# Kernel tuning notes

Hardware: AMD Instinct MI355X
Metric: run time of the kernel (lower is better)

Reference implementation:

```python
import jax, jax.numpy as jnp
import numpy as np

H = 16  # head_count
NEG = -1e18

def setup_inputs() -> dict:
    key = jax.random.key(0)
    ks = jax.random.split(key, 8)
    B, L, D = 4, 2048, 1024
    s = 1.0 / np.sqrt(D)
    return {
        "key":   jax.random.normal(ks[0], (B, L, D), jnp.float32),
        "value": jax.random.normal(ks[1], (B, L, D), jnp.float32),
        "query": jax.random.normal(ks[2], (B, L, D), jnp.float32),
        "mask":  jax.random.randint(ks[3], (B, L, L), 0, 2).astype(bool),
        "Wk": jax.random.normal(ks[4], (D, D), jnp.float32) * s,
        "bk": jnp.zeros((D,), jnp.float32),
        "Wv": jax.random.normal(ks[5], (D, D), jnp.float32) * s,
        "bv": jnp.zeros((D,), jnp.float32),
        "Wq": jax.random.normal(ks[6], (D, D), jnp.float32) * s,
        "bq": jnp.zeros((D,), jnp.float32),
        "Wo": jax.random.normal(ks[7], (D, D), jnp.float32) * s,
        "bo": jnp.zeros((D,), jnp.float32),
    }

def reference(key, value, query, mask, Wk, bk, Wv, bv, Wq, bq, Wo, bo):
    B, Lk, D = key.shape
    Lq = query.shape[1]
    dh = D // H

    def shape(x, L):  # (B, L, D) -> (B, H, L, dh)
        return x.reshape(B, L, H, dh).transpose(0, 2, 1, 3)

    k = shape(key @ Wk + bk, Lk)
    v = shape(value @ Wv + bv, Lk)
    q = shape(query @ Wq + bq, Lq) / jnp.sqrt(jnp.asarray(dh, query.dtype))

    scores = jnp.einsum('bhqd,bhkd->bhqk', q, k).astype(jnp.float32)
    scores = jnp.where(mask[:, None, :, :], NEG, scores)  # masked_fill
    attn = jax.nn.softmax(scores, axis=-1).astype(q.dtype)
    # dropout is identity at inference
    ctx = jnp.einsum('bhqk,bhkd->bhqd', attn, v)
    ctx = ctx.transpose(0, 2, 1, 3).reshape(B, Lq, D)  # unshape
    output = ctx @ Wo + bo
    top_attn = attn[:, 0, :, :]
    return (output, top_attn)
```

## Files before the change

kernel.cpp:

```cpp
#include <hip/hip_runtime.h>
#include <hip/hip_bf16.h>
#include <stdint.h>

#define Bn 4
#define Ln 2048
#define Dn 1024
#define Hn 16
#define DHn 64

typedef __attribute__((ext_vector_type(8))) short short8;
typedef __attribute__((ext_vector_type(4))) float f32x4;
typedef unsigned long long u64;
typedef __hip_bfloat16 bf16;

union U8 { uint32_t u[4]; short8 s; };

__device__ __forceinline__ short f2b(float x) {
  bf16 b = __float2bfloat16(x);
  return *(short*)&b;
}

__device__ __forceinline__ uint32_t cvt_pk_bf16(float lo, float hi) {
  uint32_t r;
  asm("v_cvt_pk_bf16_f32 %0, %1, %2" : "=v"(r) : "v"(lo), "v"(hi));
  return r;
}

__device__ __forceinline__ void gll16(const void* g, void* l) {
  __builtin_amdgcn_global_load_lds(
      (const __attribute__((address_space(1))) void*)g,
      (__attribute__((address_space(3))) void*)l, 16, 0, 0);
}

__global__ __launch_bounds__(256) void f32_to_bf16_3(
    const float* __restrict__ A, const float* __restrict__ B2, const float* __restrict__ C3,
    short* __restrict__ oA, short* __restrict__ oB, short* __restrict__ oC, int n4)
{
  const int z = blockIdx.y;
  const float* in = (z == 0) ? A : (z == 1) ? B2 : C3;
  short* out = (z == 0) ? oA : (z == 1) ? oB : oC;
  int i = blockIdx.x * 256 + threadIdx.x;
  if (i < n4) {
    float4 v = ((const float4*)in)[i];
    short4 o;
    o.x = f2b(v.x); o.y = f2b(v.y); o.z = f2b(v.z); o.w = f2b(v.w);
    ((short4*)out)[i] = o;
  }
}

__global__ __launch_bounds__(256) void transpose_w_bf16(
    const float* __restrict__ W0, const float* __restrict__ W1,
    const float* __restrict__ W2, const float* __restrict__ W3,
    short* __restrict__ WT0, short* __restrict__ WT1,
    short* __restrict__ WT2, short* __restrict__ WT3)
{
  __shared__ float t[64][65];
  const int z = blockIdx.z;
  const float* src = (z == 0) ? W0 : (z == 1) ? W1 : (z == 2) ? W2 : W3;
  short* dst = (z == 0) ? WT0 : (z == 1) ? WT1 : (z == 2) ? WT2 : WT3;
  const int tid = threadIdx.x;
  const int k0 = blockIdx.x * 64, n0 = blockIdx.y * 64;
  #pragma unroll
  for (int it = 0; it < 4; ++it) {
    int idx = it * 256 + tid;
    int row = idx >> 4, c4 = (idx & 15) * 4;
    *(float4*)&t[row][c4] = *(const float4*)&src[(size_t)(k0 + row) * Dn + n0 + c4];
  }
  __syncthreads();
  #pragma unroll
  for (int it = 0; it < 4; ++it) {
    int idx = it * 256 + tid;
    int nr = idx >> 4, kc = (idx & 15) * 4;
    short4 o;
    o.x = f2b(t[kc + 0][nr]); o.y = f2b(t[kc + 1][nr]);
    o.z = f2b(t[kc + 2][nr]); o.w = f2b(t[kc + 3][nr]);
    *(short4*)&dst[(size_t)(n0 + nr) * Dn + k0 + kc] = o;
  }
}

__global__ __launch_bounds__(256) void gemm_bias_bf16(
    const short* __restrict__ Xs, const short* __restrict__ WTs,
    const float* __restrict__ bias, void* __restrict__ Cout,
    int M, int N, int K, float scale, int mode)
{
  __shared__ short lds[2 * 128 * 32];
  short* ldsA = lds;
  short* ldsB = lds + 128 * 32;
  const int tid  = threadIdx.x;
  const int lane = tid & 63;
  const int wv   = tid >> 6;
  const int quad = lane >> 4;
  const int l16  = lane & 15;
  const int m0 = blockIdx.y * 128, n0 = blockIdx.x * 128;
  const int wm = (wv >> 1) * 64, wn = (wv & 1) * 64;

  f32x4 acc[4][4];
  #pragma unroll
  for (int i = 0; i < 4; ++i)
    #pragma unroll
    for (int j = 0; j < 4; ++j)
      acc[i][j] = (f32x4){0.f, 0.f, 0.f, 0.f};

  for (int k0 = 0; k0 < K; k0 += 32) {
    __syncthreads();
    #pragma unroll
    for (int r = 0; r < 2; ++r) {
      int idx = r * 256 + tid;
      int row = idx >> 2, kc = idx & 3;
      gll16(Xs  + (size_t)(m0 + row) * K + k0 + kc * 8, ldsA + idx * 8);
      gll16(WTs + (size_t)(n0 + row) * K + k0 + kc * 8, ldsB + idx * 8);
    }
    __syncthreads();
    short8 af[4], bfr[4];
    #pragma unroll
    for (int i = 0; i < 4; ++i)
      af[i] = *(const short8*)(ldsA + (wm + i * 16 + l16) * 32 + quad * 8);
    #pragma unroll
    for (int j = 0; j < 4; ++j)
      bfr[j] = *(const short8*)(ldsB + (wn + j * 16 + l16) * 32 + quad * 8);
    #pragma unroll
    for (int i = 0; i < 4; ++i)
      #pragma unroll
      for (int j = 0; j < 4; ++j)
        acc[i][j] = __builtin_amdgcn_mfma_f32_16x16x32_bf16(af[i], bfr[j], acc[i][j], 0, 0, 0);
  }

  if (mode == 0) {
    float* C = (float*)Cout;
    #pragma unroll
    for (int j = 0; j < 4; ++j) {
      int n = n0 + wn + j * 16 + l16;
      float bv = bias[n];
      #pragma unroll
      for (int i = 0; i < 4; ++i) {
        int mb = m0 + wm + i * 16 + quad * 4;
        #pragma unroll
        for (int r = 0; r < 4; ++r)
          C[(size_t)(mb + r) * N + n] = (acc[i][j][r] + bv) * scale;
      }
    }
  } else if (mode == 1) {
    short* C = (short*)Cout;
    #pragma unroll
    for (int j = 0; j < 4; ++j) {
      int n = n0 + wn + j * 16 + l16;
      float bv = bias[n];
      #pragma unroll
      for (int i = 0; i < 4; ++i) {
        int mb = m0 + wm + i * 16 + quad * 4;
        #pragma unroll
        for (int r = 0; r < 4; ++r)
          C[(size_t)(mb + r) * N + n] = f2b((acc[i][j][r] + bv) * scale);
      }
    }
  } else {
    short* C = (short*)Cout;
    #pragma unroll
    for (int j = 0; j < 4; ++j) {
      int n = n0 + wn + j * 16 + l16;
      float bv = bias[n];
      int hh = n >> 6, dd = n & 63;
      #pragma unroll
      for (int i = 0; i < 4; ++i) {
        int mb = m0 + wm + i * 16 + quad * 4;
        int bb = mb >> 11, ll = mb & 2047;
        short4 o;
        o.x = f2b((acc[i][j][0] + bv) * scale);
        o.y = f2b((acc[i][j][1] + bv) * scale);
        o.z = f2b((acc[i][j][2] + bv) * scale);
        o.w = f2b((acc[i][j][3] + bv) * scale);
        *(short4*)&C[((size_t)(bb * 16 + hh) * 64 + dd) * 2048 + ll] = o;
      }
    }
  }
}

__global__ __launch_bounds__(256) void pack_mask(const int* __restrict__ mask, u64* __restrict__ pm)
{
  size_t tg = (size_t)blockIdx.x * 256 + threadIdx.x;
  int v = mask[tg];
  u64 bal = __ballot(v != 0);
  if ((threadIdx.x & 63) == 0) pm[tg >> 6] = bal;
}


__device__ __forceinline__ const short8* ldsfrag(const short* lds, int row, int colb) {
  return (const short8*)((const char*)lds + row * 128 + (colb ^ ((row & 7) << 4)));
}

__global__ __launch_bounds__(256) void attn_fused(
    const short* __restrict__ qb, const short* __restrict__ kb,
    const short* __restrict__ vT, const u64* __restrict__ pm,
    short* __restrict__ ctx_bf, float* __restrict__ topattn)
{
  __shared__ short ldsK[64 * 64];
  __shared__ short ldsVT[64 * 64];
  const int tid  = threadIdx.x;
  const int lane = tid & 63, wv = tid >> 6;
  const int quad = lane >> 4, l16 = lane & 15;
  const int b = blockIdx.z, h = blockIdx.y, q0 = blockIdx.x * 64;
  const int q_g = q0 + wv * 16 + l16;

  const short* qrow = qb + (size_t)(b * Ln + q_g) * Dn + h * DHn;
  short8 qf[2];
  qf[0] = *(const short8*)(qrow + quad * 8);
  qf[1] = *(const short8*)(qrow + 32 + quad * 8);

  const u64* pmq = pm + (size_t)(b * Ln + q_g) * 32;
  const short* kbase = kb + (size_t)b * Ln * Dn + h * DHn;
  const short* vbase = vT + (size_t)(b * Hn + h) * DHn * Ln;

  float m_r = -INFINITY, l_r = 0.f;
  f32x4 oc[4];
  #pragma unroll
  for (int dt = 0; dt < 4; ++dt) oc[dt] = (f32x4){0.f, 0.f, 0.f, 0.f};

  const int srcA = ((lane >> 4) & 1) * 32 + l16;
  const int srcB = srcA + 16;
  const bool hiHalf = (lane & 32) != 0;

  for (int k0 = 0; k0 < Ln; k0 += 64) {
    __syncthreads();
    #pragma unroll
    for (int it = 0; it < 2; ++it) {
      int idx = it * 256 + tid;
      int row = idx >> 3, cb = (idx & 7) * 16;
      int scb = cb ^ ((row & 7) << 4);
      gll16(kbase + (size_t)(k0 + row) * Dn + (scb >> 1), ldsK + idx * 8);
      gll16(vbase + (size_t)row * Ln + k0 + (scb >> 1), ldsVT + idx * 8);
    }
    __syncthreads();

    f32x4 sv[4];
    #pragma unroll
    for (int mt = 0; mt < 4; ++mt) sv[mt] = (f32x4){0.f, 0.f, 0.f, 0.f};
    #pragma unroll
    for (int s = 0; s < 2; ++s)
      #pragma unroll
      for (int mt = 0; mt < 4; ++mt) {
        short8 kf = *ldsfrag(ldsK, mt * 16 + l16, s * 64 + quad * 16);
        sv[mt] = __builtin_amdgcn_mfma_f32_16x16x32_bf16(kf, qf[s], sv[mt], 0, 0, 0);
      }

    u64 w = pmq[k0 >> 6];
    float ps[4][4];
    float tm = -INFINITY;
    #pragma unroll
    for (int mt = 0; mt < 4; ++mt)
      #pragma unroll
      for (int r = 0; r < 4; ++r) {
        int kl = mt * 16 + quad * 4 + r;
        float s = ((w >> kl) & 1ull) ? -INFINITY : sv[mt][r];
        ps[mt][r] = s;
        tm = fmaxf(tm, s);
      }
    tm = fmaxf(tm, __shfl_xor(tm, 16, 64));
    tm = fmaxf(tm, __shfl_xor(tm, 32, 64));
    if (tm > m_r + 8.f) {
      float sc = __expf(m_r - tm);
      l_r *= sc;
      #pragma unroll
      for (int dt = 0; dt < 4; ++dt)
        #pragma unroll
        for (int r = 0; r < 4; ++r) oc[dt][r] *= sc;
      m_r = tm;
    }
    float ls = 0.f;
    #pragma unroll
    for (int mt = 0; mt < 4; ++mt)
      #pragma unroll
      for (int r = 0; r < 4; ++r) {
        float p = __expf(ps[mt][r] - m_r);
        ps[mt][r] = p;
        ls += p;
      }
    l_r += ls;

    uint32_t d0[4], d1[4];
    #pragma unroll
    for (int mt = 0; mt < 4; ++mt) {
      d0[mt] = cvt_pk_bf16(ps[mt][0], ps[mt][1]);
      d1[mt] = cvt_pk_bf16(ps[mt][2], ps[mt][3]);
    }

    #pragma unroll
    for (int ks = 0; ks < 2; ++ks) {
      uint32_t a0  = (uint32_t)__shfl((int)d0[2 * ks],     srcA, 64);
      uint32_t a0b = (uint32_t)__shfl((int)d0[2 * ks + 1], srcA, 64);
      uint32_t a1  = (uint32_t)__shfl((int)d1[2 * ks],     srcA, 64);
      uint32_t a1b = (uint32_t)__shfl((int)d1[2 * ks + 1], srcA, 64);
      uint32_t b0  = (uint32_t)__shfl((int)d0[2 * ks],     srcB, 64);
      uint32_t b0b = (uint32_t)__shfl((int)d0[2 * ks + 1], srcB, 64);
      uint32_t b1  = (uint32_t)__shfl((int)d1[2 * ks],     srcB, 64);
      uint32_t b1b = (uint32_t)__shfl((int)d1[2 * ks + 1], srcB, 64);
      U8 u;
      u.u[0] = hiHalf ? a0b : a0;
      u.u[1] = hiHalf ? a1b : a1;
      u.u[2] = hiHalf ? b0b : b0;
      u.u[3] = hiHalf ? b1b : b1;
      short8 pf = u.s;
      #pragma unroll
      for (int dt = 0; dt < 4; ++dt) {
        short8 vf = *ldsfrag(ldsVT, dt * 16 + l16, ks * 64 + quad * 16);
        oc[dt] = __builtin_amdgcn_mfma_f32_16x16x32_bf16(vf, pf, oc[dt], 0, 0, 0);
      }
    }
  }

  l_r += __shfl_xor(l_r, 16, 64);
  l_r += __shfl_xor(l_r, 32, 64);
  const float rinv = (l_r > 0.f) ? 1.f / l_r : 0.f;

  short* crow = ctx_bf + (size_t)(b * Ln + q_g) * Dn + h * DHn;
  #pragma unroll
  for (int dt = 0; dt < 4; ++dt) {
    short4 o;
    o.x = f2b(oc[dt][0] * rinv); o.y = f2b(oc[dt][1] * rinv);
    o.z = f2b(oc[dt][2] * rinv); o.w = f2b(oc[dt][3] * rinv);
    *(short4*)&crow[dt * 16 + quad * 4] = o;
  }

  if (h == 0) {
    float* tpb = topattn + (size_t)(b * Ln + q_g) * Ln;
    for (int k0 = 0; k0 < Ln; k0 += 64) {
      __syncthreads();
      #pragma unroll
      for (int it = 0; it < 2; ++it) {
        int idx = it * 256 + tid;
        int row = idx >> 3, cb = (idx & 7) * 16;
        int scb = cb ^ ((row & 7) << 4);
        gll16(kbase + (size_t)(k0 + row) * Dn + (scb >> 1), ldsK + idx * 8);
      }
      __syncthreads();
      f32x4 sv[4];
      #pragma unroll
      for (int mt = 0; mt < 4; ++mt) sv[mt] = (f32x4){0.f, 0.f, 0.f, 0.f};
      #pragma unroll
      for (int s = 0; s < 2; ++s)
        #pragma unroll
        for (int mt = 0; mt < 4; ++mt) {
          short8 kf = *ldsfrag(ldsK, mt * 16 + l16, s * 64 + quad * 16);
          sv[mt] = __builtin_amdgcn_mfma_f32_16x16x32_bf16(kf, qf[s], sv[mt], 0, 0, 0);
        }
      u64 w = pmq[k0 >> 6];
      #pragma unroll
      for (int mt = 0; mt < 4; ++mt)
        #pragma unroll
        for (int r = 0; r < 4; ++r) {
          int kl = mt * 16 + quad * 4 + r;
          float p = ((w >> kl) & 1ull) ? 0.f : __expf(sv[mt][r] - m_r) * rinv;
          tpb[k0 + kl] = p;
        }
    }
  }
}

extern "C" void kernel_launch(void* const* d_in, const int* in_sizes, int n_in,
                              void* d_out, int out_size, void* d_ws, size_t ws_size,
                              hipStream_t stream) {
  (void)in_sizes; (void)n_in; (void)out_size; (void)ws_size;
  const float* key   = (const float*)d_in[0];
  const float* value = (const float*)d_in[1];
  const float* query = (const float*)d_in[2];
  const int*   mask  = (const int*)d_in[3];
  const float* Wk = (const float*)d_in[4];
  const float* bk = (const float*)d_in[5];
  const float* Wv = (const float*)d_in[6];
  const float* bv = (const float*)d_in[7];
  const float* Wq = (const float*)d_in[8];
  const float* bq = (const float*)d_in[9];
  const float* Wo = (const float*)d_in[10];
  const float* bo = (const float*)d_in[11];

  char* ws = (char*)d_ws;
  const size_t MiB = 1ull << 20;
  short* kc  = (short*)(ws +   0 * MiB);
  short* vc  = (short*)(ws +  16 * MiB);
  short* qc  = (short*)(ws +  32 * MiB);
  short* WkT = (short*)(ws +  48 * MiB);
  short* WvT = (short*)(ws +  50 * MiB);
  short* WqT = (short*)(ws +  52 * MiB);
  short* WoT = (short*)(ws +  54 * MiB);
  short* qb  = (short*)(ws +  56 * MiB);
  short* kb  = (short*)(ws +  72 * MiB);
  short* vT  = (short*)(ws +  88 * MiB);
  u64*   pm  = (u64*)  (ws + 104 * MiB);
  short* ctx_bf = (short*)(ws + 106 * MiB);

  float* out     = (float*)d_out;
  float* topattn = out + (size_t)Bn * Ln * Dn;

  const int M = Bn * Ln;
  const int n4 = (M * Dn) / 4;

  f32_to_bf16_3<<<dim3(n4 / 256, 3), 256, 0, stream>>>(key, value, query, kc, vc, qc, n4);
  transpose_w_bf16<<<dim3(16, 16, 4), 256, 0, stream>>>(Wk, Wv, Wq, Wo, WkT, WvT, WqT, WoT);

  gemm_bias_bf16<<<dim3(8, 64), 256, 0, stream>>>(kc, WkT, bk, kb, M, Dn, Dn, 1.0f,   1);
  gemm_bias_bf16<<<dim3(8, 64), 256, 0, stream>>>(vc, WvT, bv, vT, M, Dn, Dn, 1.0f,   2);
  gemm_bias_bf16<<<dim3(8, 64), 256, 0, stream>>>(qc, WqT, bq, qb, M, Dn, Dn, 0.125f, 1);

  pack_mask<<<dim3((Bn * Ln * Ln) / 256), 256, 0, stream>>>(mask, pm);

  attn_fused<<<dim3(Ln / 64, Hn, Bn), 256, 0, stream>>>(qb, kb, vT, pm, ctx_bf, topattn);

  gemm_bias_bf16<<<dim3(8, 64), 256, 0, stream>>>(ctx_bf, WoT, bo, out, M, Dn, Dn, 1.0f, 0);
}
```

Before: 593.6 us.

## Double-buffer GEMM and attention loads, fuse QKV GEMMs, inline top-attn write

The GEMM core and the attention kernel now double-buffer their LDS tiles, prefetching the next K-slice while computing the current one, and raise wave priority around MFMA blocks. The three QKV projections become one launch with a z dimension. The head-0 second pass that recomputed scores for top_attn is removed: probabilities are written during the main pass with per-tile maxima, and a small fix-up kernel rescales them by the final max and normalizer. The attention grid is remapped to a 1D swizzle that groups heads and batches. This costs extra LDS, a small extra kernel, and an extra read-modify-write over the top_attn buffer.

```diff
diff --git a/kernel.cpp b/kernel.cpp
--- a/kernel.cpp
+++ b/kernel.cpp
@@ -78,14 +78,12 @@
   }
 }
 
-__global__ __launch_bounds__(256) void gemm_bias_bf16(
+__device__ __forceinline__ void gemm_core(
     const short* __restrict__ Xs, const short* __restrict__ WTs,
     const float* __restrict__ bias, void* __restrict__ Cout,
     int M, int N, int K, float scale, int mode)
 {
-  __shared__ short lds[2 * 128 * 32];
-  short* ldsA = lds;
-  short* ldsB = lds + 128 * 32;
+  __shared__ short lds[2][2 * 128 * 32];
   const int tid  = threadIdx.x;
   const int lane = tid & 63;
   const int wv   = tid >> 6;
@@ -101,16 +99,30 @@
     for (int j = 0; j < 4; ++j)
       acc[i][j] = (f32x4){0.f, 0.f, 0.f, 0.f};
 
-  for (int k0 = 0; k0 < K; k0 += 32) {
-    __syncthreads();
-    #pragma unroll
-    for (int r = 0; r < 2; ++r) {
-      int idx = r * 256 + tid;
-      int row = idx >> 2, kc = idx & 3;
-      gll16(Xs  + (size_t)(m0 + row) * K + k0 + kc * 8, ldsA + idx * 8);
-      gll16(WTs + (size_t)(n0 + row) * K + k0 + kc * 8, ldsB + idx * 8);
-    }
-    __syncthreads();
+  #pragma unroll
+  for (int r = 0; r < 2; ++r) {
+    int idx = r * 256 + tid;
+    int row = idx >> 2, kc = idx & 3;
+    gll16(Xs  + (size_t)(m0 + row) * K + kc * 8, &lds[0][idx * 8]);
+    gll16(WTs + (size_t)(n0 + row) * K + kc * 8, &lds[0][128 * 32 + idx * 8]);
+  }
+  __syncthreads();
+
+  const int NT = K >> 5;
+  int cur = 0;
+  for (int t = 0; t < NT; ++t) {
+    if (t + 1 < NT) {
+      const int kn = (t + 1) * 32;
+      #pragma unroll
+      for (int r = 0; r < 2; ++r) {
+        int idx = r * 256 + tid;
+        int row = idx >> 2, kc = idx & 3;
+        gll16(Xs  + (size_t)(m0 + row) * K + kn + kc * 8, &lds[cur ^ 1][idx * 8]);
+        gll16(WTs + (size_t)(n0 + row) * K + kn + kc * 8, &lds[cur ^ 1][128 * 32 + idx * 8]);
+      }
+    }
+    const short* ldsA = lds[cur];
+    const short* ldsB = lds[cur] + 128 * 32;
     short8 af[4], bfr[4];
     #pragma unroll
     for (int i = 0; i < 4; ++i)
@@ -118,11 +130,15 @@
     #pragma unroll
     for (int j = 0; j < 4; ++j)
       bfr[j] = *(const short8*)(ldsB + (wn + j * 16 + l16) * 32 + quad * 8);
+    __builtin_amdgcn_s_setprio(1);
     #pragma unroll
     for (int i = 0; i < 4; ++i)
       #pragma unroll
       for (int j = 0; j < 4; ++j)
         acc[i][j] = __builtin_amdgcn_mfma_f32_16x16x32_bf16(af[i], bfr[j], acc[i][j], 0, 0, 0);
+    __builtin_amdgcn_s_setprio(0);
+    __syncthreads();
+    cur ^= 1;
   }
 
   if (mode == 0) {
@@ -175,6 +191,29 @@
   }
 }
 
+__global__ __launch_bounds__(256) void gemm_qkv(
+    const short* __restrict__ kc, const short* __restrict__ vc, const short* __restrict__ qc,
+    const short* __restrict__ WkT, const short* __restrict__ WvT, const short* __restrict__ WqT,
+    const float* __restrict__ bk, const float* __restrict__ bv, const float* __restrict__ bq,
+    short* __restrict__ kb, short* __restrict__ vT, short* __restrict__ qb2)
+{
+  const int z = blockIdx.z;
+  const short* Xs = (z == 0) ? kc : (z == 1) ? vc : qc;
+  const short* WT = (z == 0) ? WkT : (z == 1) ? WvT : WqT;
+  const float* bs = (z == 0) ? bk : (z == 1) ? bv : bq;
+  void* C = (z == 0) ? (void*)kb : (z == 1) ? (void*)vT : (void*)qb2;
+  float scale = (z == 2) ? 0.125f : 1.0f;
+  int mode = (z == 1) ? 2 : 1;
+  gemm_core(Xs, WT, bs, C, Bn * Ln, Dn, Dn, scale, mode);
+}
+
+__global__ __launch_bounds__(256) void gemm_wo(
+    const short* __restrict__ ctx, const short* __restrict__ WoT,
+    const float* __restrict__ bo, float* __restrict__ out)
+{
+  gemm_core(ctx, WoT, bo, out, Bn * Ln, Dn, Dn, 1.0f, 0);
+}
+
 __global__ __launch_bounds__(256) void pack_mask(const int* __restrict__ mask, u64* __restrict__ pm)
 {
   size_t tg = (size_t)blockIdx.x * 256 + threadIdx.x;
@@ -191,14 +230,19 @@
 __global__ __launch_bounds__(256) void attn_fused(
     const short* __restrict__ qb, const short* __restrict__ kb,
     const short* __restrict__ vT, const u64* __restrict__ pm,
-    short* __restrict__ ctx_bf, float* __restrict__ topattn)
-{
-  __shared__ short ldsK[64 * 64];
-  __shared__ short ldsVT[64 * 64];
+    short* __restrict__ ctx_bf, float* __restrict__ topattn,
+    float* __restrict__ mtile, float2* __restrict__ stat2)
+{
+  __shared__ short ldsK[2][64 * 64];
+  __shared__ short ldsVT[2][64 * 64];
   const int tid  = threadIdx.x;
   const int lane = tid & 63, wv = tid >> 6;
   const int quad = lane >> 4, l16 = lane & 15;
-  const int b = blockIdx.z, h = blockIdx.y, q0 = blockIdx.x * 64;
+  const int g = blockIdx.x;
+  const int x = (g >> 3) & 31;
+  const int c = (g & 7) + ((g >> 8) << 3);
+  const int h = c & 15, b = c >> 4;
+  const int q0 = x * 64;
   const int q_g = q0 + wv * 16 + l16;
 
   const short* qrow = qb + (size_t)(b * Ln + q_g) * Dn + h * DHn;
@@ -210,6 +254,16 @@
   const short* kbase = kb + (size_t)b * Ln * Dn + h * DHn;
   const short* vbase = vT + (size_t)(b * Hn + h) * DHn * Ln;
 
+  #pragma unroll
+  for (int it = 0; it < 2; ++it) {
+    int idx = it * 256 + tid;
+    int row = idx >> 3, cb = (idx & 7) * 16;
+    int scb = cb ^ ((row & 7) << 4);
+    gll16(kbase + (size_t)row * Dn + (scb >> 1), &ldsK[0][idx * 8]);
+    gll16(vbase + (size_t)row * Ln + (scb >> 1), &ldsVT[0][idx * 8]);
+  }
+  __syncthreads();
+
   float m_r = -INFINITY, l_r = 0.f;
   f32x4 oc[4];
   #pragma unroll
@@ -219,41 +273,38 @@
   const int srcB = srcA + 16;
   const bool hiHalf = (lane & 32) != 0;
 
-  for (int k0 = 0; k0 < Ln; k0 += 64) {
-    __syncthreads();
-    #pragma unroll
-    for (int it = 0; it < 2; ++it) {
-      int idx = it * 256 + tid;
-      int row = idx >> 3, cb = (idx & 7) * 16;
-      int scb = cb ^ ((row & 7) << 4);
-      gll16(kbase + (size_t)(k0 + row) * Dn + (scb >> 1), ldsK + idx * 8);
-      gll16(vbase + (size_t)row * Ln + k0 + (scb >> 1), ldsVT + idx * 8);
-    }
-    __syncthreads();
+  int cur = 0;
+  for (int t = 0; t < 32; ++t) {
+    const int k0 = t * 64;
+    if (t < 31) {
+      const int kn = k0 + 64;
+      #pragma unroll
+      for (int it = 0; it < 2; ++it) {
+        int idx = it * 256 + tid;
+        int row = idx >> 3, cb = (idx & 7) * 16;
+        int scb = cb ^ ((row & 7) << 4);
+        gll16(kbase + (size_t)(kn + row) * Dn + (scb >> 1), &ldsK[cur ^ 1][idx * 8]);
+        gll16(vbase + (size_t)row * Ln + kn + (scb >> 1), &ldsVT[cur ^ 1][idx * 8]);
+      }
+    }
 
     f32x4 sv[4];
     #pragma unroll
     for (int mt = 0; mt < 4; ++mt) sv[mt] = (f32x4){0.f, 0.f, 0.f, 0.f};
+    __builtin_amdgcn_s_setprio(1);
     #pragma unroll
     for (int s = 0; s < 2; ++s)
       #pragma unroll
       for (int mt = 0; mt < 4; ++mt) {
-        short8 kf = *ldsfrag(ldsK, mt * 16 + l16, s * 64 + quad * 16);
+        short8 kf = *ldsfrag(&ldsK[cur][0], mt * 16 + l16, s * 64 + quad * 16);
         sv[mt] = __builtin_amdgcn_mfma_f32_16x16x32_bf16(kf, qf[s], sv[mt], 0, 0, 0);
       }
-
-    u64 w = pmq[k0 >> 6];
-    float ps[4][4];
-    float tm = -INFINITY;
-    #pragma unroll
-    for (int mt = 0; mt < 4; ++mt)
-      #pragma unroll
-      for (int r = 0; r < 4; ++r) {
-        int kl = mt * 16 + quad * 4 + r;
-        float s = ((w >> kl) & 1ull) ? -INFINITY : sv[mt][r];
-        ps[mt][r] = s;
-        tm = fmaxf(tm, s);
-      }
+    __builtin_amdgcn_s_setprio(0);
+
+    float tm = fmaxf(fmaxf(sv[0][0], sv[0][1]), fmaxf(sv[0][2], sv[0][3]));
+    #pragma unroll
+    for (int mt = 1; mt < 4; ++mt)
+      tm = fmaxf(tm, fmaxf(fmaxf(sv[mt][0], sv[mt][1]), fmaxf(sv[mt][2], sv[mt][3])));
     tm = fmaxf(tm, __shfl_xor(tm, 16, 64));
     tm = fmaxf(tm, __shfl_xor(tm, 32, 64));
     if (tm > m_r + 8.f) {
@@ -265,22 +316,34 @@
         for (int r = 0; r < 4; ++r) oc[dt][r] *= sc;
       m_r = tm;
     }
+    const u64 w = pmq[t];
     float ls = 0.f;
     #pragma unroll
-    for (int mt = 0; mt < 4; ++mt)
+    for (int mt = 0; mt < 4; ++mt) {
+      unsigned nib = (unsigned)(w >> (mt * 16 + quad * 4)) & 0xFu;
       #pragma unroll
       for (int r = 0; r < 4; ++r) {
-        float p = __expf(ps[mt][r] - m_r);
-        ps[mt][r] = p;
+        float p = __expf(sv[mt][r] - m_r);
+        p = (nib & (1u << r)) ? 0.f : p;
+        sv[mt][r] = p;
         ls += p;
       }
+    }
     l_r += ls;
 
+    if (h == 0) {
+      float* tpb = topattn + (size_t)(b * Ln + q_g) * Ln + k0 + quad * 4;
+      #pragma unroll
+      for (int mt = 0; mt < 4; ++mt)
+        *(float4*)&tpb[mt * 16] = *(float4*)&sv[mt];
+      if (quad == 0) mtile[(size_t)(b * Ln + q_g) * 32 + t] = m_r;
+    }
+
     uint32_t d0[4], d1[4];
     #pragma unroll
     for (int mt = 0; mt < 4; ++mt) {
-      d0[mt] = cvt_pk_bf16(ps[mt][0], ps[mt][1]);
-      d1[mt] = cvt_pk_bf16(ps[mt][2], ps[mt][3]);
+      d0[mt] = cvt_pk_bf16(sv[mt][0], sv[mt][1]);
+      d1[mt] = cvt_pk_bf16(sv[mt][2], sv[mt][3]);
     }
 
     #pragma unroll
@@ -299,12 +362,16 @@
       u.u[2] = hiHalf ? b0b : b0;
       u.u[3] = hiHalf ? b1b : b1;
       short8 pf = u.s;
+      __builtin_amdgcn_s_setprio(1);
       #pragma unroll
       for (int dt = 0; dt < 4; ++dt) {
-        short8 vf = *ldsfrag(ldsVT, dt * 16 + l16, ks * 64 + quad * 16);
+        short8 vf = *ldsfrag(&ldsVT[cur][0], dt * 16 + l16, ks * 64 + quad * 16);
         oc[dt] = __builtin_amdgcn_mfma_f32_16x16x32_bf16(vf, pf, oc[dt], 0, 0, 0);
       }
-    }
+      __builtin_amdgcn_s_setprio(0);
+    }
+    __syncthreads();
+    cur ^= 1;
   }
 
   l_r += __shfl_xor(l_r, 16, 64);
@@ -319,40 +386,23 @@
     o.z = f2b(oc[dt][2] * rinv); o.w = f2b(oc[dt][3] * rinv);
     *(short4*)&crow[dt * 16 + quad * 4] = o;
   }
-
-  if (h == 0) {
-    float* tpb = topattn + (size_t)(b * Ln + q_g) * Ln;
-    for (int k0 = 0; k0 < Ln; k0 += 64) {
-      __syncthreads();
-      #pragma unroll
-      for (int it = 0; it < 2; ++it) {
-        int idx = it * 256 + tid;
-        int row = idx >> 3, cb = (idx & 7) * 16;
-        int scb = cb ^ ((row & 7) << 4);
-        gll16(kbase + (size_t)(k0 + row) * Dn + (scb >> 1), ldsK + idx * 8);
-      }
-      __syncthreads();
-      f32x4 sv[4];
-      #pragma unroll
-      for (int mt = 0; mt < 4; ++mt) sv[mt] = (f32x4){0.f, 0.f, 0.f, 0.f};
-      #pragma unroll
-      for (int s = 0; s < 2; ++s)
-        #pragma unroll
-        for (int mt = 0; mt < 4; ++mt) {
-          short8 kf = *ldsfrag(ldsK, mt * 16 + l16, s * 64 + quad * 16);
-          sv[mt] = __builtin_amdgcn_mfma_f32_16x16x32_bf16(kf, qf[s], sv[mt], 0, 0, 0);
-        }
-      u64 w = pmq[k0 >> 6];
-      #pragma unroll
-      for (int mt = 0; mt < 4; ++mt)
-        #pragma unroll
-        for (int r = 0; r < 4; ++r) {
-          int kl = mt * 16 + quad * 4 + r;
-          float p = ((w >> kl) & 1ull) ? 0.f : __expf(sv[mt][r] - m_r) * rinv;
-          tpb[k0 + kl] = p;
-        }
-    }
-  }
+  if (h == 0 && quad == 0)
+    stat2[b * Ln + q_g] = make_float2(m_r, rinv);
+}
+
+__global__ __launch_bounds__(256) void topattn_fix(
+    float* __restrict__ topattn, const float* __restrict__ mtile,
+    const float2* __restrict__ stat2)
+{
+  const int row = blockIdx.x;
+  const float2 st = stat2[row];
+  const int tid = threadIdx.x;
+  const float sc = __expf(mtile[(size_t)row * 32 + (tid >> 3)] - st.x) * st.y;
+  float4* p = (float4*)(topattn + (size_t)row * Ln) + tid * 2;
+  float4 a = p[0], b2 = p[1];
+  a.x *= sc; a.y *= sc; a.z *= sc; a.w *= sc;
+  b2.x *= sc; b2.y *= sc; b2.z *= sc; b2.w *= sc;
+  p[0] = a; p[1] = b2;
 }
 
 extern "C" void kernel_launch(void* const* d_in, const int* in_sizes, int n_in,
@@ -386,6 +436,8 @@
   short* vT  = (short*)(ws +  88 * MiB);
   u64*   pm  = (u64*)  (ws + 104 * MiB);
   short* ctx_bf = (short*)(ws + 106 * MiB);
+  float* mtile  = (float*)(ws + 122 * MiB);
+  float2* stat2 = (float2*)(ws + 123 * MiB);
 
   float* out     = (float*)d_out;
   float* topattn = out + (size_t)Bn * Ln * Dn;
@@ -396,13 +448,12 @@
   f32_to_bf16_3<<<dim3(n4 / 256, 3), 256, 0, stream>>>(key, value, query, kc, vc, qc, n4);
   transpose_w_bf16<<<dim3(16, 16, 4), 256, 0, stream>>>(Wk, Wv, Wq, Wo, WkT, WvT, WqT, WoT);
 
-  gemm_bias_bf16<<<dim3(8, 64), 256, 0, stream>>>(kc, WkT, bk, kb, M, Dn, Dn, 1.0f,   1);
-  gemm_bias_bf16<<<dim3(8, 64), 256, 0, stream>>>(vc, WvT, bv, vT, M, Dn, Dn, 1.0f,   2);
-  gemm_bias_bf16<<<dim3(8, 64), 256, 0, stream>>>(qc, WqT, bq, qb, M, Dn, Dn, 0.125f, 1);
+  gemm_qkv<<<dim3(8, 64, 3), 256, 0, stream>>>(kc, vc, qc, WkT, WvT, WqT, bk, bv, bq, kb, vT, qb);
 
   pack_mask<<<dim3((Bn * Ln * Ln) / 256), 256, 0, stream>>>(mask, pm);
 
-  attn_fused<<<dim3(Ln / 64, Hn, Bn), 256, 0, stream>>>(qb, kb, vT, pm, ctx_bf, topattn);
-
-  gemm_bias_bf16<<<dim3(8, 64), 256, 0, stream>>>(ctx_bf, WoT, bo, out, M, Dn, Dn, 1.0f, 0);
-}
+  attn_fused<<<dim3(2048), 256, 0, stream>>>(qb, kb, vT, pm, ctx_bf, topattn, mtile, stat2);
+  topattn_fix<<<dim3(Bn * Ln), 256, 0, stream>>>(topattn, mtile, stat2);
+
+  gemm_wo<<<dim3(8, 64), 256, 0, stream>>>(ctx_bf, WoT, bo, out);
+}
```

Measured after the change: 564.7 us. -4.9%, faster.
